# Kernel optimization log

Hardware: AMD Instinct MI355X
Metric: run time of the kernel (lower is better)

Reference implementation:

```python
import jax, jax.numpy as jnp
import numpy as np

W_DIM = 512
IN_CH = 512
OUT_CH = 512
K = 3
PAD = K // 2
LR_MUL = 1.0
WEIGHT_GAIN = LR_MUL / np.sqrt(IN_CH * K * K)
MOD_WEIGHT_GAIN = 1.0 / np.sqrt(W_DIM)  # EqualizedLinear lr_mul=1.0
MOD_BIAS_GAIN = 1.0


def setup_inputs() -> dict:
    key = jax.random.key(0)
    k1, k2, k3, k4 = jax.random.split(key, 4)
    x = jax.random.normal(k1, (16, IN_CH, 64, 64), dtype=jnp.float32)
    w = jax.random.normal(k2, (16, W_DIM), dtype=jnp.float32)
    weight = jax.random.normal(k3, (OUT_CH, IN_CH, K, K), dtype=jnp.float32) / LR_MUL
    mod_weight = jax.random.normal(k4, (IN_CH, W_DIM), dtype=jnp.float32)
    mod_bias = jnp.ones((IN_CH,), dtype=jnp.float32)  # bias_init=1.0
    return {"x": x, "w": w, "weight": weight, "mod_weight": mod_weight, "mod_bias": mod_bias}


def _conv_one(xi, wi):
    # xi: [C_in, H, W], wi: [C_out, C_in, K, K]
    out = jax.lax.conv_general_dilated(
        xi[None], wi, window_strides=(1, 1),
        padding=[(PAD, PAD), (PAD, PAD)],
        dimension_numbers=("NCHW", "OIHW", "NCHW"))
    return out[0]


def reference(x, w, weight, mod_weight, mod_bias):
    # style = EqualizedLinear(w): [B, C_in]
    style = w @ (mod_weight * MOD_WEIGHT_GAIN).T + mod_bias * MOD_BIAS_GAIN
    # modulate weights per-sample: [B, C_out, C_in, K, K]
    wmod = (weight * WEIGHT_GAIN)[None] * style[:, None, :, None, None]
    # demodulate
    demod = jax.lax.rsqrt(jnp.sum(jnp.square(wmod), axis=(2, 3, 4), keepdims=True) + 1e-8)
    wmod = wmod * demod
    # per-sample conv (groups=batch in the original) via vmap
    out = jax.vmap(_conv_one)(x, wmod)  # [B, C_out, H, W]
    return out
```

## Files before the change

### kernel.cpp

```cpp
#include <hip/hip_runtime.h>
#include <hip/hip_bf16.h>

#define IN_CH 512
#define OUT_CH 512
#define HW 64
#define BATCH 16
#define WEIGHT_GAIN 0.014731391274719739f
#define MOD_WEIGHT_GAIN 0.04419417382415922f

#define PAD_W 66
#define XS_PIX_STRIDE 512

typedef __attribute__((ext_vector_type(8))) short frag8;
typedef __attribute__((ext_vector_type(4))) float f32x4;

__global__ void style_kernel(const float* __restrict__ w, const float* __restrict__ mw,
                             const float* __restrict__ mb, float* __restrict__ style) {
    const int gw = (blockIdx.x * 256 + threadIdx.x) >> 6;
    const int lane = threadIdx.x & 63;
    const int b = gw >> 9;
    const int i = gw & 511;
    const float4* mwp = (const float4*)(mw + (size_t)i * 512 + lane * 8);
    const float4* wp  = (const float4*)(w + (size_t)b * 512 + lane * 8);
    float4 m0 = mwp[0], m1 = mwp[1];
    float4 w0 = wp[0],  w1 = wp[1];
    float s = m0.x * w0.x + m0.y * w0.y + m0.z * w0.z + m0.w * w0.w
            + m1.x * w1.x + m1.y * w1.y + m1.z * w1.z + m1.w * w1.w;
#pragma unroll
    for (int off = 32; off > 0; off >>= 1) s += __shfl_down(s, off, 64);
    if (lane == 0) style[(size_t)b * 512 + i] = s * MOD_WEIGHT_GAIN + mb[i];
}

__global__ void wprep_kernel(const float* __restrict__ weight, float* __restrict__ wsq,
                             __hip_bfloat16* __restrict__ wbf) {
    const int idx = blockIdx.x * 256 + threadIdx.x;
    const float* wp = weight + idx * 9;
    float s = 0.f;
#pragma unroll
    for (int kk = 0; kk < 9; ++kk) {
        float v = wp[kk];
        s += v * v;
        wbf[kk * 262144 + idx] = __float2bfloat16(v);
    }
    wsq[idx] = s * (WEIGHT_GAIN * WEIGHT_GAIN);
}

__global__ void demod_kernel(const float* __restrict__ style, const float* __restrict__ wsq,
                             float* __restrict__ sc) {
    const int gw = (blockIdx.x * 256 + threadIdx.x) >> 6;
    const int lane = threadIdx.x & 63;
    const int b = gw >> 9;
    const int o = gw & 511;
    const float4* wq = (const float4*)(wsq + (size_t)o * 512 + lane * 8);
    const float4* st = (const float4*)(style + (size_t)b * 512 + lane * 8);
    float4 q0 = wq[0], q1 = wq[1];
    float4 s0 = st[0], s1 = st[1];
    float acc = q0.x * s0.x * s0.x + q0.y * s0.y * s0.y + q0.z * s0.z * s0.z + q0.w * s0.w * s0.w
              + q1.x * s1.x * s1.x + q1.y * s1.y * s1.y + q1.z * s1.z * s1.z + q1.w * s1.w * s1.w;
#pragma unroll
    for (int off = 32; off > 0; off >>= 1) acc += __shfl_down(acc, off, 64);
    if (lane == 0) sc[(size_t)b * 512 + o] = rsqrtf(acc + 1e-8f) * WEIGHT_GAIN;
}

__global__ void xs_kernel(const float* __restrict__ x, const float* __restrict__ style,
                          __hip_bfloat16* __restrict__ xsp) {
    const int b = blockIdx.z;
    const int t = threadIdx.x;
    if (blockIdx.x == 64) {
        const int g = blockIdx.y;
        const int wv = t >> 6, lane = t & 63;
        for (int k = wv; k < 65; k += 4) {
            const int p = g * 65 + k;
            int row, col;
            if (p < 66)       { row = 0;            col = p; }
            else if (p < 132) { row = 65;           col = p - 66; }
            else if (p < 196) { row = p - 132 + 1;  col = 0; }
            else              { row = p - 196 + 1;  col = 65; }
            uint4* dst = (uint4*)(xsp + (((size_t)b * PAD_W + row) * PAD_W + col) * XS_PIX_STRIDE);
            dst[lane] = uint4{0, 0, 0, 0};
        }
        return;
    }
    const int y = blockIdx.x;
    const int lane = t & 63;
    const int j0 = (blockIdx.y * 4 + (t >> 6)) * 32;

    const float* xb = x + (((size_t)b * 512 + j0) * 64 + y) * 64 + lane;
    const float* stb = style + (size_t)b * 512 + j0;
    __hip_bfloat16* dst = xsp + (((size_t)b * PAD_W + (y + 1)) * PAD_W + (lane + 1)) * XS_PIX_STRIDE + j0;

    union { __hip_bfloat16 h[32]; uint4 u[4]; } pk;
#pragma unroll
    for (int k = 0; k < 32; ++k) {
        float v = xb[(size_t)k * 4096];
        pk.h[k] = __float2bfloat16(v * stb[k]);
    }
#pragma unroll
    for (int q = 0; q < 4; ++q) ((uint4*)dst)[q] = pk.u[q];
}

__global__ __launch_bounds__(512, 1) void conv_kernel(const __hip_bfloat16* __restrict__ wbf,
                            const __hip_bfloat16* __restrict__ xsp,
                            const float* __restrict__ sc,
                            float* __restrict__ out) {
    __shared__ char lds[131072];

    const int bid = blockIdx.x;
    const int logical = (bid & 7) * 64 + (bid >> 3);
    const int m0 = (logical & 1) << 8;
    const int pt = (logical >> 1) & 15;
    const int b  = logical >> 5;
    const int p0 = pt << 8;
    const int y0 = pt << 2;
    const int t = threadIdx.x;

    const int r_base = t >> 3;
    const int s_slot = (t & 7) ^ (r_base & 7);
    int pixoff[4];
#pragma unroll
    for (int i = 0; i < 4; ++i) {
        const int ri = i * 64 + r_base;
        const int yy = y0 + (ri >> 6);
        const int xx = ri & 63;
        pixoff[i] = (((b * PAD_W) + yy) * PAD_W + xx) * XS_PIX_STRIDE + s_slot * 8;
    }

    const int wv = t >> 6;
    const int wm = (wv >> 2) * 128;
    const int wn = (wv & 3) * 64;
    const int lane = t & 63;
    const int ln15 = lane & 15;
    const int quad = lane >> 4;

    f32x4 acc[8][4] = {};
    frag8 bfr[4][2];
    frag8 af[4];
    frag8 ag[8];

#define LDSADDR(P) ((unsigned)(unsigned long)(__attribute__((address_space(3))) const char*)(P))
#define DSREAD(DST, ADDR) asm volatile("ds_read_b128 %0, %1" : "=v"(DST) : "v"(ADDR))

#define GLL(SRC, DST) __builtin_amdgcn_global_load_lds(                               \
    (const __attribute__((address_space(1))) unsigned int*)(SRC),                     \
    (__attribute__((address_space(3))) unsigned int*)(DST), 16, 0, 0)

#define STAGE_A(J, HALF) do {                                                         \
    const int jA_ = (J);                                                              \
    const __hip_bfloat16* srcA_ = wbf + (jA_ >> 3) * 262144                           \
        + (size_t)(m0 + (HALF) * 128 + r_base) * 512 + ((jA_ & 7) << 6) + s_slot * 8; \
    char* dstA_ = lds + (jA_ & 1) * 65536 + (HALF) * 16384 + t * 16;                  \
    GLL(srcA_, dstA_);                                                                \
    GLL(srcA_ + 64 * 512, dstA_ + 8192);                                              \
} while (0)

#define STAGE_B(J, HALF) do {                                                         \
    const int jB_ = (J);                                                              \
    const int kkB_ = jB_ >> 3;                                                        \
    const __hip_bfloat16* srcB_ = xsp + ((kkB_ / 3) * PAD_W + (kkB_ % 3)) * XS_PIX_STRIDE \
        + ((jB_ & 7) << 6);                                                           \
    char* dstB_ = lds + (jB_ & 1) * 65536 + 32768 + (HALF) * 16384 + t * 16;          \
    GLL(srcB_ + pixoff[(HALF) * 2 + 0], dstB_);                                       \
    GLL(srcB_ + pixoff[(HALF) * 2 + 1], dstB_ + 8192);                                \
} while (0)

#define RD_B_ALL(CUR) do {                                                            \
    const char* Bp_ = lds + (CUR) * 65536 + 32768;                                    \
    _Pragma("unroll")                                                                 \
    for (int nt = 0; nt < 4; ++nt) {                                                  \
        const int R_ = wn + nt * 16 + ln15;                                           \
        _Pragma("unroll")                                                             \
        for (int ks = 0; ks < 2; ++ks) {                                              \
            const unsigned a_ = LDSADDR(Bp_ + R_ * 128 + (((ks * 4 + quad) ^ (R_ & 7)) << 4)); \
            DSREAD(bfr[nt][ks], a_);                                                  \
        }                                                                             \
    }                                                                                 \
} while (0)

#define RD_A4(CUR, KS, MTH, DST) do {                                                 \
    const char* Ap_ = lds + (CUR) * 65536;                                            \
    _Pragma("unroll")                                                                 \
    for (int mt = 0; mt < 4; ++mt) {                                                  \
        const int R_ = wm + ((MTH) * 4 + mt) * 16 + ln15;                             \
        const unsigned a_ = LDSADDR(Ap_ + R_ * 128 + ((((KS) * 4 + quad) ^ (R_ & 7)) << 4)); \
        DSREAD((DST)[mt], a_);                                                        \
    }                                                                                 \
} while (0)

#define MFMA_Q(AF, MTH, KS) do {                                                      \
    __builtin_amdgcn_s_setprio(1);                                                    \
    _Pragma("unroll")                                                                 \
    for (int mt = 0; mt < 4; ++mt)                                                    \
        _Pragma("unroll")                                                             \
        for (int nt = 0; nt < 4; ++nt)                                                \
            acc[(MTH) * 4 + mt][nt] = __builtin_amdgcn_mfma_f32_16x16x32_bf16(        \
                (AF)[mt], bfr[nt][(KS)], acc[(MTH) * 4 + mt][nt], 0, 0, 0);           \
    __builtin_amdgcn_s_setprio(0);                                                    \
} while (0)

#define BAR asm volatile("s_barrier" ::: "memory")
#define LG8 asm volatile("s_waitcnt lgkmcnt(8)" ::: "memory")
#define LGKM0 do { asm volatile("s_waitcnt lgkmcnt(0)" ::: "memory");                 \
                   __builtin_amdgcn_sched_barrier(0); } while (0)
#define VM6 asm volatile("s_waitcnt vmcnt(6)" ::: "memory")
#define VM0 asm volatile("s_waitcnt vmcnt(0)" ::: "memory")

#define KTILE(J, CUR, SP1, SP2, VMC) do {                                             \
                                  \
    RD_B_ALL(CUR);                                                                    \
    RD_A4(CUR, 0, 0, af);                                                             \
    if (SP1) STAGE_A((J) + 1, 1);                                                     \
    LG8; BAR; LGKM0; MFMA_Q(af, 0, 0); BAR;                                           \
                                                  \
    RD_A4(CUR, 0, 1, af);                                                             \
    if (SP2) STAGE_B((J) + 2, 0);                                                     \
    BAR; LGKM0; MFMA_Q(af, 1, 0); BAR;                                                \
                                                  \
    RD_A4(CUR, 1, 0, ag);                                                             \
    RD_A4(CUR, 1, 1, ag + 4);                                                         \
    if (SP2) STAGE_B((J) + 2, 1);                                                     \
    BAR; LGKM0; MFMA_Q(ag, 0, 1); BAR;                                                \
                                                               \
    if (SP2) STAGE_A((J) + 2, 0);                                                     \
    VMC; BAR; MFMA_Q(ag + 4, 1, 1); BAR;                                              \
} while (0)

    STAGE_B(0, 0); STAGE_B(0, 1); STAGE_A(0, 0); STAGE_A(0, 1);
    STAGE_B(1, 0); STAGE_B(1, 1); STAGE_A(1, 0);
    VM6; BAR;

    for (int j = 0; j < 70; j += 2) {
        KTILE(j, 0, 1, 1, VM6);
        KTILE(j + 1, 1, 1, 1, VM6);
    }
    KTILE(70, 0, 1, 0, VM0);
    KTILE(71, 1, 0, 0, (void)0);

#undef KTILE
#undef VM0
#undef VM6
#undef LGKM0
#undef LG8
#undef BAR
#undef MFMA_Q
#undef RD_A4
#undef RD_B_ALL
#undef STAGE_B
#undef STAGE_A
#undef GLL
#undef DSREAD
#undef LDSADDR

    const float* scb = sc + b * 512;
    float* outb = out + (size_t)b * 512 * 4096;
#pragma unroll
    for (int mt = 0; mt < 8; ++mt) {
        const int mrow = m0 + wm + mt * 16 + quad * 4;
#pragma unroll
        for (int v = 0; v < 4; ++v) {
            const float sv = scb[mrow + v];
            float* orow = outb + (size_t)(mrow + v) * 4096 + p0 + wn + ln15;
#pragma unroll
            for (int nt = 0; nt < 4; ++nt)
                orow[nt * 16] = acc[mt][nt][v] * sv;
        }
    }
}

extern "C" void kernel_launch(void* const* d_in, const int* in_sizes, int n_in,
                              void* d_out, int out_size, void* d_ws, size_t ws_size,
                              hipStream_t stream) {
    (void)in_sizes; (void)n_in; (void)out_size; (void)ws_size;
    const float* x      = (const float*)d_in[0];
    const float* w      = (const float*)d_in[1];
    const float* weight = (const float*)d_in[2];
    const float* mw     = (const float*)d_in[3];
    const float* mb     = (const float*)d_in[4];
    float* out = (float*)d_out;

    char* ws = (char*)d_ws;
    float* style         = (float*)(ws + 0);
    float* sc            = (float*)(ws + 32768);
    float* wsq           = (float*)(ws + 65536);
    __hip_bfloat16* wbf  = (__hip_bfloat16*)(ws + 1114112);
    __hip_bfloat16* xsp  = (__hip_bfloat16*)(ws + 5832704);

    wprep_kernel<<<dim3(1024), dim3(256), 0, stream>>>(weight, wsq, wbf);
    style_kernel<<<dim3(2048), dim3(256), 0, stream>>>(w, mw, mb, style);
    demod_kernel<<<dim3(2048), dim3(256), 0, stream>>>(style, wsq, sc);
    xs_kernel<<<dim3(65, 4, BATCH), dim3(256), 0, stream>>>(x, style, xsp);
    conv_kernel<<<dim3(512), dim3(512), 0, stream>>>(wbf, xsp, sc, out);
}
```

Baseline: 508.7 us.

## Software-pipeline LDS fragment reads one MFMA quarter ahead with partial waits

Result: slower. 520.0 us (+2.2%).

```diff
diff --git a/kernel.cpp b/kernel.cpp
--- a/kernel.cpp
+++ b/kernel.cpp
@@ -135,7 +135,7 @@
     f32x4 acc[8][4] = {};
     frag8 bfr[4][2];
     frag8 af[4];
-    frag8 ag[8];
+    frag8 ag[4];
 
 #define LDSADDR(P) ((unsigned)(unsigned long)(__attribute__((address_space(3))) const char*)(P))
 #define DSREAD(DST, ADDR) asm volatile("ds_read_b128 %0, %1" : "=v"(DST) : "v"(ADDR))
@@ -163,16 +163,13 @@
     GLL(srcB_ + pixoff[(HALF) * 2 + 1], dstB_ + 8192);                                \
 } while (0)
 
-#define RD_B_ALL(CUR) do {                                                            \
+#define RD_B4(CUR, KS) do {                                                           \
     const char* Bp_ = lds + (CUR) * 65536 + 32768;                                    \
     _Pragma("unroll")                                                                 \
     for (int nt = 0; nt < 4; ++nt) {                                                  \
         const int R_ = wn + nt * 16 + ln15;                                           \
-        _Pragma("unroll")                                                             \
-        for (int ks = 0; ks < 2; ++ks) {                                              \
-            const unsigned a_ = LDSADDR(Bp_ + R_ * 128 + (((ks * 4 + quad) ^ (R_ & 7)) << 4)); \
-            DSREAD(bfr[nt][ks], a_);                                                  \
-        }                                                                             \
+        const unsigned a_ = LDSADDR(Bp_ + R_ * 128 + ((((KS) * 4 + quad) ^ (R_ & 7)) << 4)); \
+        DSREAD(bfr[nt][(KS)], a_);                                                    \
     }                                                                                 \
 } while (0)
 
@@ -198,52 +195,62 @@
 } while (0)
 
 #define BAR asm volatile("s_barrier" ::: "memory")
-#define LG8 asm volatile("s_waitcnt lgkmcnt(8)" ::: "memory")
-#define LGKM0 do { asm volatile("s_waitcnt lgkmcnt(0)" ::: "memory");                 \
-                   __builtin_amdgcn_sched_barrier(0); } while (0)
-#define VM6 asm volatile("s_waitcnt vmcnt(6)" ::: "memory")
+#define SB0 __builtin_amdgcn_sched_barrier(0)
+#define LGW(N) asm volatile("s_waitcnt lgkmcnt(" #N ")" ::: "memory")
+#define VM4 asm volatile("s_waitcnt vmcnt(4)" ::: "memory")
 #define VM0 asm volatile("s_waitcnt vmcnt(0)" ::: "memory")
-
-#define KTILE(J, CUR, SP1, SP2, VMC) do {                                             \
-                                  \
-    RD_B_ALL(CUR);                                                                    \
-    RD_A4(CUR, 0, 0, af);                                                             \
-    if (SP1) STAGE_A((J) + 1, 1);                                                     \
-    LG8; BAR; LGKM0; MFMA_Q(af, 0, 0); BAR;                                           \
-                                                  \
-    RD_A4(CUR, 0, 1, af);                                                             \
-    if (SP2) STAGE_B((J) + 2, 0);                                                     \
-    BAR; LGKM0; MFMA_Q(af, 1, 0); BAR;                                                \
-                                                  \
-    RD_A4(CUR, 1, 0, ag);                                                             \
-    RD_A4(CUR, 1, 1, ag + 4);                                                         \
-    if (SP2) STAGE_B((J) + 2, 1);                                                     \
-    BAR; LGKM0; MFMA_Q(ag, 0, 1); BAR;                                                \
-                                                               \
-    if (SP2) STAGE_A((J) + 2, 0);                                                     \
-    VMC; BAR; MFMA_Q(ag + 4, 1, 1); BAR;                                              \
+#define VMNONE do {} while (0)
+
+#define TILE(J, CUR, NXT, SA1, SB2, SA2, VMW, LAST) do {                              \
+                          \
+    BAR;                                                                              \
+    RD_A4(CUR, 0, 1, ag);                                                             \
+    RD_B4(CUR, 1);                                                                    \
+    if (SA1) STAGE_A((J) + 1, 1);                                                     \
+    LGW(8); SB0; MFMA_Q(af, 0, 0);                                                    \
+                                      \
+    BAR;                                                                              \
+    RD_A4(CUR, 1, 0, af);                                                             \
+    if (SB2) STAGE_B((J) + 2, 0);                                                     \
+    LGW(4); SB0; MFMA_Q(ag, 1, 0);                                                    \
+                                      \
+    BAR;                                                                              \
+    RD_A4(CUR, 1, 1, ag);                                                             \
+    if (SB2) STAGE_B((J) + 2, 1);                                                     \
+    LGW(4); SB0; MFMA_Q(af, 0, 1);                                                    \
+                    \
+    VMW;                                                                              \
+    BAR;                                                                              \
+    if (!(LAST)) { RD_A4(NXT, 0, 0, af); RD_B4(NXT, 0); }                             \
+    if (SA2) STAGE_A((J) + 2, 0);                                                     \
+    if (!(LAST)) { LGW(8); } else { LGW(0); }                                         \
+    SB0; MFMA_Q(ag, 1, 1);                                                            \
 } while (0)
 
     STAGE_B(0, 0); STAGE_B(0, 1); STAGE_A(0, 0); STAGE_A(0, 1);
     STAGE_B(1, 0); STAGE_B(1, 1); STAGE_A(1, 0);
-    VM6; BAR;
+    asm volatile("s_waitcnt vmcnt(6)" ::: "memory");
+    BAR;
+    RD_A4(0, 0, 0, af);
+    RD_B4(0, 0);
 
     for (int j = 0; j < 70; j += 2) {
-        KTILE(j, 0, 1, 1, VM6);
-        KTILE(j + 1, 1, 1, 1, VM6);
-    }
-    KTILE(70, 0, 1, 0, VM0);
-    KTILE(71, 1, 0, 0, (void)0);
-
-#undef KTILE
+        TILE(j,     0, 1, 1, 1, 1, VM4, 0);
+        TILE(j + 1, 1, 0, 1, 1, 1, VM4, 0);
+    }
+    TILE(70, 0, 1, 1, 0, 0, VM0, 0);
+    TILE(71, 1, 0, 0, 0, 0, VMNONE, 1);
+
+#undef TILE
+#undef VMNONE
 #undef VM0
-#undef VM6
-#undef LGKM0
-#undef LG8
+#undef VM4
+#undef LGW
+#undef SB0
 #undef BAR
 #undef MFMA_Q
 #undef RD_A4
-#undef RD_B_ALL
+#undef RD_B4
 #undef STAGE_B
 #undef STAGE_A
 #undef GLL
```
